# Kernel tuning notes

Hardware: AMD Instinct MI355X
Metric: run time of the kernel (lower is better)

Reference implementation:

```python
import jax, jax.numpy as jnp
import numpy as np

N = 262144          # nodes
F_NODE, F_EDGE = 64, 16
OUT = [64, 64, 64]  # hidden sizes per layer / readout fingerprint size
TARGET = 12
N_DEG = 4           # d = [1,2,3,4]
IN0 = F_NODE + F_EDGE   # duvenaud message out size, layer 0
IN1 = OUT[0] + F_EDGE   # layer 1


def _build_graph():
    # ring: (i, i+1 mod N) -> every node degree 2
    ring = np.stack([np.arange(N), (np.arange(N) + 1) % N], 1)
    # chords: (2i, 2i + N//2) for i < N//8 -> distinct endpoints, bumps degree to 3
    i = np.arange(N // 8)
    chords = np.stack([2 * i, 2 * i + N // 2], 1)
    und = np.concatenate([ring, chords], 0)            # [E, 2] undirected edges
    E = und.shape[0]
    # directed (both directions) for message passing
    src = np.concatenate([und[:, 0], und[:, 1]]).astype(np.int64)
    dst = np.concatenate([und[:, 1], und[:, 0]]).astype(np.int64)
    eid = np.concatenate([np.arange(E), np.arange(E)]).astype(np.int64)
    deg = np.bincount(np.concatenate([und[:, 0], und[:, 1]]), minlength=N)
    deg_idx = (deg - 1).astype(np.int64)               # index into d=[1,2,3,4]
    return src, dst, eid, deg_idx, E


def setup_inputs() -> dict:
    key = jax.random.key(0)
    ks = jax.random.split(key, 9)
    src, dst, eid, deg_idx, E = _build_graph()
    s0 = 1.0 / np.sqrt(IN0)
    sR = 1.0 / np.sqrt(OUT[0])
    return {
        "h_in": jax.random.normal(ks[0], (N, F_NODE), jnp.float32),
        "edge_feat": jax.random.normal(ks[1], (E, F_EDGE), jnp.float32),
        "U0": jax.random.normal(ks[2], (N_DEG, IN0, OUT[0]), jnp.float32) * s0,
        "U1": jax.random.normal(ks[3], (N_DEG, IN1, OUT[1]), jnp.float32) * s0,
        "R0": jax.random.normal(ks[4], (F_NODE, OUT[2]), jnp.float32) * sR,
        "R1": jax.random.normal(ks[5], (OUT[0], OUT[2]), jnp.float32) * sR,
        "R2": jax.random.normal(ks[6], (OUT[1], OUT[2]), jnp.float32) * sR,
        "W_out": jax.random.normal(ks[7], (OUT[2], TARGET), jnp.float32) * sR,
        "b_out": jax.random.normal(ks[8], (TARGET,), jnp.float32) * 0.01,
        "edge_src": jnp.asarray(src),
        "edge_dst": jnp.asarray(dst),
        "edge_eid": jnp.asarray(eid),
        "deg_idx": jnp.asarray(deg_idx),
    }


def reference(h_in, edge_feat, U0, U1, R0, R1, R2, W_out, b_out,
              edge_src, edge_dst, edge_eid, deg_idx):
    ef = edge_feat[edge_eid]  # [2E, F_EDGE] directed-edge features

    def step(h, U):
        # duvenaud message: m_{v<-w} = concat(h_w, e_vw); sum over neighbors
        m = jnp.concatenate([h[edge_src], ef], axis=1)              # [2E, in]
        m_agg = jax.ops.segment_sum(m, edge_dst, num_segments=N)    # [N, in]
        # duvenaud update: h_v' = sigmoid(W_{deg(v)} m_v)
        out_all = jnp.einsum('ni,dio->ndo', m_agg, U)               # [N, D, out]
        sel = jnp.take_along_axis(out_all, deg_idx[:, None, None], axis=1)[:, 0, :]
        return jax.nn.sigmoid(sel)

    h1 = step(h_in, U0)
    h2 = step(h1, U1)
    # duvenaud readout: sum over layers & nodes of softmax(h_l @ R_l), then linear
    fp = (jax.nn.softmax(h_in @ R0, axis=-1)
          + jax.nn.softmax(h1 @ R1, axis=-1)
          + jax.nn.softmax(h2 @ R2, axis=-1)).sum(axis=0)           # [OUT[2]]
    return fp @ W_out + b_out                                       # [TARGET]
```

## Files before the change

### kernel.cpp

```cpp
#include <hip/hip_runtime.h>
#include <stdint.h>

#define NN 262144
#define VMASK (NN - 1)
#define GRID_NODES (NN / 64)

typedef __attribute__((ext_vector_type(8))) short short8;
typedef __attribute__((ext_vector_type(4))) float f32x4;

__device__ __forceinline__ float bf2f(uint16_t h) {
    union { uint32_t u; float f; } a; a.u = ((uint32_t)h) << 16; return a.f;
}
__device__ __forceinline__ uint16_t f2bf(float x) {
    union { float f; uint32_t u; } a; a.f = x;
    uint32_t r = a.u + 0x7fffu + ((a.u >> 16) & 1u);
    return (uint16_t)(r >> 16);
}
__device__ __forceinline__ float sigm(float x) { return 1.f / (1.f + __expf(-x)); }

__device__ __forceinline__ void chord_of(int v, int& cn, int& ce) {
    cn = -1; ce = -1;
    if ((v & 1) == 0) {
        if (v < NN / 4)                            { cn = v + NN / 2; ce = NN + (v >> 1); }
        else if (v >= NN / 2 && v < (3 * NN) / 4)  { cn = v - NN / 2; ce = NN + ((v - NN / 2) >> 1); }
    }
}

__global__ void prep_weights(const float* __restrict__ U0, const float* __restrict__ U1,
                             const float* __restrict__ R0, const float* __restrict__ R1,
                             const float* __restrict__ R2,
                             uint16_t* __restrict__ Ut0, uint16_t* __restrict__ Ut1,
                             uint16_t* __restrict__ Rt)
{
    int idx = blockIdx.x * 256 + threadIdx.x;
    if (idx < 10240) {
        int o = idx / 160, k = idx - o * 160;
        float v = (k < 80) ? U0[5120 + k * 64 + o] : U0[2 * 5120 + (k - 80) * 64 + o];
        Ut0[o * 160 + k] = f2bf(v);
    } else if (idx < 20480) {
        int r = idx - 10240;
        int o = r / 160, k = r - o * 160;
        float v = (k < 80) ? U1[5120 + k * 64 + o] : U1[2 * 5120 + (k - 80) * 64 + o];
        Ut1[o * 160 + k] = f2bf(v);
    } else if (idx < 20480 + 3 * 4096) {
        int r = idx - 20480;
        int layer = r >> 12;
        int e = r & 4095;
        int o = e >> 6, i = e & 63;
        const float* R = (layer == 0) ? R0 : ((layer == 1) ? R1 : R2);
        Rt[layer * 4096 + o * 64 + i] = f2bf(R[i * 64 + o]);
    }
}

template<int MODE>
__global__ __launch_bounds__(256, 4) void fused_layer(
    const float* __restrict__ hf, const uint16_t* __restrict__ hb,
    const float* __restrict__ ef,
    const uint16_t* __restrict__ Ut, const uint16_t* __restrict__ RtA,
    const uint16_t* __restrict__ Rt0, uint16_t* __restrict__ hout,
    float* __restrict__ fpacc)
{
    __shared__ alignas(16) uint16_t B[64][168];
    __shared__ alignas(16) uint16_t X[64][72];
    __shared__ float partial[4][64];

    const int t = threadIdx.x, w = t >> 6, l = t & 63;
    const int bid = blockIdx.x;
    const int chunk = ((bid & 7) << 9) + (bid >> 3);
    const int vb = chunk * 64;
    const int row16 = l & 15, cq = l >> 4, koff = cq * 8;
    const int v = vb + w * 16 + row16;
    const short8 zz = {0, 0, 0, 0, 0, 0, 0, 0};

#pragma unroll
    for (int it = t; it < 1280; it += 256) {
        int o = it / 20, c = it - o * 20;
        *(short8*)&B[o][c * 8] = *(const short8*)(Ut + o * 160 + c * 8);
    }

    const int vm1 = (v - 1) & VMASK, vp1 = (v + 1) & VMASK;
    const int e1 = vm1;
    int cn, ce; chord_of(v, cn, ce);
    const int off = (cn >= 0) ? 80 : 0;
    short8 afr[5];
#pragma unroll
    for (int ks = 0; ks < 5; ++ks) {
        const int mk = ks * 32 + koff - off;
        short8 r = zz;
        if (mk >= 0 && mk < 64) {
            float s[8];
            if (MODE == 0) {
                const float4* x4 = (const float4*)(hf + (size_t)vm1 * 64 + mk);
                const float4* y4 = (const float4*)(hf + (size_t)vp1 * 64 + mk);
                float4 x0 = x4[0], x1 = x4[1], y0 = y4[0], y1 = y4[1];
                s[0] = x0.x + y0.x; s[1] = x0.y + y0.y; s[2] = x0.z + y0.z; s[3] = x0.w + y0.w;
                s[4] = x1.x + y1.x; s[5] = x1.y + y1.y; s[6] = x1.z + y1.z; s[7] = x1.w + y1.w;
                if (cn >= 0) {
                    const float4* z4 = (const float4*)(hf + (size_t)cn * 64 + mk);
                    float4 z0 = z4[0], z1 = z4[1];
                    s[0] += z0.x; s[1] += z0.y; s[2] += z0.z; s[3] += z0.w;
                    s[4] += z1.x; s[5] += z1.y; s[6] += z1.z; s[7] += z1.w;
                }
            } else {
                short8 x = *(const short8*)(hb + (size_t)vm1 * 64 + mk);
                short8 y = *(const short8*)(hb + (size_t)vp1 * 64 + mk);
#pragma unroll
                for (int j = 0; j < 8; ++j) s[j] = bf2f((uint16_t)x[j]) + bf2f((uint16_t)y[j]);
                if (cn >= 0) {
                    short8 zv = *(const short8*)(hb + (size_t)cn * 64 + mk);
#pragma unroll
                    for (int j = 0; j < 8; ++j) s[j] += bf2f((uint16_t)zv[j]);
                }
            }
#pragma unroll
            for (int j = 0; j < 8; ++j) r[j] = (short)f2bf(s[j]);
        } else if (mk >= 64 && mk < 80) {
            const int ek = mk - 64;
            const float4* p4 = (const float4*)(ef + (size_t)e1 * 16 + ek);
            const float4* q4 = (const float4*)(ef + (size_t)v * 16 + ek);
            float4 p0 = p4[0], p1 = p4[1], q0 = q4[0], q1 = q4[1];
            float s[8] = { p0.x + q0.x, p0.y + q0.y, p0.z + q0.z, p0.w + q0.w,
                           p1.x + q1.x, p1.y + q1.y, p1.z + q1.z, p1.w + q1.w };
            if (ce >= 0) {
                const float4* c4 = (const float4*)(ef + (size_t)ce * 16 + ek);
                float4 c0 = c4[0], c1 = c4[1];
                s[0] += c0.x; s[1] += c0.y; s[2] += c0.z; s[3] += c0.w;
                s[4] += c1.x; s[5] += c1.y; s[6] += c1.z; s[7] += c1.w;
            }
#pragma unroll
            for (int j = 0; j < 8; ++j) r[j] = (short)f2bf(s[j]);
        }
        afr[ks] = r;
    }

    short8 h0f0 = zz, h0f1 = zz;
    if (MODE == 0) {
        const float4* s4 = (const float4*)(hf + (size_t)v * 64);
        float4 a0 = s4[cq * 2], a1 = s4[cq * 2 + 1];
        float4 b0v = s4[8 + cq * 2], b1v = s4[8 + cq * 2 + 1];
        h0f0[0] = (short)f2bf(a0.x); h0f0[1] = (short)f2bf(a0.y);
        h0f0[2] = (short)f2bf(a0.z); h0f0[3] = (short)f2bf(a0.w);
        h0f0[4] = (short)f2bf(a1.x); h0f0[5] = (short)f2bf(a1.y);
        h0f0[6] = (short)f2bf(a1.z); h0f0[7] = (short)f2bf(a1.w);
        h0f1[0] = (short)f2bf(b0v.x); h0f1[1] = (short)f2bf(b0v.y);
        h0f1[2] = (short)f2bf(b0v.z); h0f1[3] = (short)f2bf(b0v.w);
        h0f1[4] = (short)f2bf(b1v.x); h0f1[5] = (short)f2bf(b1v.y);
        h0f1[6] = (short)f2bf(b1v.z); h0f1[7] = (short)f2bf(b1v.w);
    }

    __syncthreads();

    const int bc = row16;
    {
        f32x4 acc0 = {0,0,0,0}, acc1 = {0,0,0,0}, acc2 = {0,0,0,0}, acc3 = {0,0,0,0};
#pragma unroll
        for (int ks = 0; ks < 5; ++ks) {
            const int kk = ks * 32 + koff;
            short8 a  = afr[ks];
            short8 b0 = *(const short8*)&B[bc][kk];
            short8 b1 = *(const short8*)&B[16 + bc][kk];
            short8 b2 = *(const short8*)&B[32 + bc][kk];
            short8 b3 = *(const short8*)&B[48 + bc][kk];
            acc0 = __builtin_amdgcn_mfma_f32_16x16x32_bf16(a, b0, acc0, 0, 0, 0);
            acc1 = __builtin_amdgcn_mfma_f32_16x16x32_bf16(a, b1, acc1, 0, 0, 0);
            acc2 = __builtin_amdgcn_mfma_f32_16x16x32_bf16(a, b2, acc2, 0, 0, 0);
            acc3 = __builtin_amdgcn_mfma_f32_16x16x32_bf16(a, b3, acc3, 0, 0, 0);
        }
        const int row0 = w * 16 + cq * 4;
#pragma unroll
        for (int r = 0; r < 4; ++r) {
            X[row0 + r][row16]      = f2bf(sigm(acc0[r]));
            X[row0 + r][16 + row16] = f2bf(sigm(acc1[r]));
            X[row0 + r][32 + row16] = f2bf(sigm(acc2[r]));
            X[row0 + r][48 + row16] = f2bf(sigm(acc3[r]));
        }
    }
    __syncthreads();

#pragma unroll
    for (int it = t; it < 512; it += 256) {
        int o = it >> 3, c = it & 7;
        *(short8*)&B[o][c * 8] = *(const short8*)(RtA + o * 64 + c * 8);
    }
    if (MODE == 0) {
#pragma unroll
        for (int it = t; it < 512; it += 256) {
            int o = it >> 3, c = it & 7;
            *(short8*)&B[o][72 + c * 8] = *(const short8*)(Rt0 + o * 64 + c * 8);
        }
#pragma unroll
        for (int it = t; it < 512; it += 256) {
            int row = it >> 3, c = it & 7;
            *(short8*)(hout + (size_t)(vb + row) * 64 + c * 8) = *(const short8*)&X[row][c * 8];
        }
    }
    __syncthreads();

    float ca0 = 0.f, ca1 = 0.f, ca2 = 0.f, ca3 = 0.f;
    const int ar = w * 16 + row16;
    {
        f32x4 acc0 = {0,0,0,0}, acc1 = {0,0,0,0}, acc2 = {0,0,0,0}, acc3 = {0,0,0,0};
#pragma unroll
        for (int ks = 0; ks < 2; ++ks) {
            const int kk = ks * 32 + koff;
            short8 a  = *(const short8*)&X[ar][kk];
            short8 b0 = *(const short8*)&B[bc][kk];
            short8 b1 = *(const short8*)&B[16 + bc][kk];
            short8 b2 = *(const short8*)&B[32 + bc][kk];
            short8 b3 = *(const short8*)&B[48 + bc][kk];
            acc0 = __builtin_amdgcn_mfma_f32_16x16x32_bf16(a, b0, acc0, 0, 0, 0);
            acc1 = __builtin_amdgcn_mfma_f32_16x16x32_bf16(a, b1, acc1, 0, 0, 0);
            acc2 = __builtin_amdgcn_mfma_f32_16x16x32_bf16(a, b2, acc2, 0, 0, 0);
            acc3 = __builtin_amdgcn_mfma_f32_16x16x32_bf16(a, b3, acc3, 0, 0, 0);
        }
#pragma unroll
        for (int r = 0; r < 4; ++r) {
            float z0 = acc0[r], z1 = acc1[r], z2 = acc2[r], z3 = acc3[r];
            float m = fmaxf(fmaxf(z0, z1), fmaxf(z2, z3));
            m = fmaxf(m, __shfl_xor(m, 1)); m = fmaxf(m, __shfl_xor(m, 2));
            m = fmaxf(m, __shfl_xor(m, 4)); m = fmaxf(m, __shfl_xor(m, 8));
            float e0 = __expf(z0 - m), e1v = __expf(z1 - m), e2 = __expf(z2 - m), e3 = __expf(z3 - m);
            float s = e0 + e1v + e2 + e3;
            s += __shfl_xor(s, 1); s += __shfl_xor(s, 2);
            s += __shfl_xor(s, 4); s += __shfl_xor(s, 8);
            const float inv = 1.f / s;
            ca0 += e0 * inv; ca1 += e1v * inv; ca2 += e2 * inv; ca3 += e3 * inv;
        }
    }
    if (MODE == 0) {
        f32x4 acc0 = {0,0,0,0}, acc1 = {0,0,0,0}, acc2 = {0,0,0,0}, acc3 = {0,0,0,0};
#pragma unroll
        for (int ks = 0; ks < 2; ++ks) {
            const int kk = ks * 32 + koff;
            short8 a  = (ks == 0) ? h0f0 : h0f1;
            short8 b0 = *(const short8*)&B[bc][72 + kk];
            short8 b1 = *(const short8*)&B[16 + bc][72 + kk];
            short8 b2 = *(const short8*)&B[32 + bc][72 + kk];
            short8 b3 = *(const short8*)&B[48 + bc][72 + kk];
            acc0 = __builtin_amdgcn_mfma_f32_16x16x32_bf16(a, b0, acc0, 0, 0, 0);
            acc1 = __builtin_amdgcn_mfma_f32_16x16x32_bf16(a, b1, acc1, 0, 0, 0);
            acc2 = __builtin_amdgcn_mfma_f32_16x16x32_bf16(a, b2, acc2, 0, 0, 0);
            acc3 = __builtin_amdgcn_mfma_f32_16x16x32_bf16(a, b3, acc3, 0, 0, 0);
        }
#pragma unroll
        for (int r = 0; r < 4; ++r) {
            float z0 = acc0[r], z1 = acc1[r], z2 = acc2[r], z3 = acc3[r];
            float m = fmaxf(fmaxf(z0, z1), fmaxf(z2, z3));
            m = fmaxf(m, __shfl_xor(m, 1)); m = fmaxf(m, __shfl_xor(m, 2));
            m = fmaxf(m, __shfl_xor(m, 4)); m = fmaxf(m, __shfl_xor(m, 8));
            float e0 = __expf(z0 - m), e1v = __expf(z1 - m), e2 = __expf(z2 - m), e3 = __expf(z3 - m);
            float s = e0 + e1v + e2 + e3;
            s += __shfl_xor(s, 1); s += __shfl_xor(s, 2);
            s += __shfl_xor(s, 4); s += __shfl_xor(s, 8);
            const float inv = 1.f / s;
            ca0 += e0 * inv; ca1 += e1v * inv; ca2 += e2 * inv; ca3 += e3 * inv;
        }
    }

    ca0 += __shfl_xor(ca0, 16); ca0 += __shfl_xor(ca0, 32);
    ca1 += __shfl_xor(ca1, 16); ca1 += __shfl_xor(ca1, 32);
    ca2 += __shfl_xor(ca2, 16); ca2 += __shfl_xor(ca2, 32);
    ca3 += __shfl_xor(ca3, 16); ca3 += __shfl_xor(ca3, 32);
    if (cq == 0) {
        partial[w][l]      = ca0;
        partial[w][16 + l] = ca1;
        partial[w][32 + l] = ca2;
        partial[w][48 + l] = ca3;
    }
    __syncthreads();
    if (t < 64)
        atomicAdd(&fpacc[((bid & 7) << 6) + t],
                  partial[0][t] + partial[1][t] + partial[2][t] + partial[3][t]);
}

__global__ void final_kernel(const float* __restrict__ fpacc, const float* __restrict__ W,
                             const float* __restrict__ b, float* __restrict__ out)
{
    __shared__ float ft[64];
    const int t = threadIdx.x;
    if (t < 64) {
        float s = 0.f;
#pragma unroll
        for (int k = 0; k < 8; ++k) s += fpacc[k * 64 + t];
        ft[t] = s;
    }
    __syncthreads();
    if (t < 12) {
        float s = b[t];
#pragma unroll 8
        for (int j = 0; j < 64; ++j) s += ft[j] * W[j * 12 + t];
        out[t] = s;
    }
}

extern "C" void kernel_launch(void* const* d_in, const int* in_sizes, int n_in,
                              void* d_out, int out_size, void* d_ws, size_t ws_size,
                              hipStream_t stream)
{
    const float* h_in = (const float*)d_in[0];
    const float* ef   = (const float*)d_in[1];
    const float* U0   = (const float*)d_in[2];
    const float* U1   = (const float*)d_in[3];
    const float* R0   = (const float*)d_in[4];
    const float* R1   = (const float*)d_in[5];
    const float* R2   = (const float*)d_in[6];
    const float* W    = (const float*)d_in[7];
    const float* bo   = (const float*)d_in[8];

    uint16_t* h1  = (uint16_t*)d_ws;
    uint16_t* Ut0 = h1 + (size_t)NN * 64;
    uint16_t* Ut1 = Ut0 + 10240;
    uint16_t* Rt  = Ut1 + 10240;
    float* fpacc  = (float*)(Rt + 3 * 4096);

    hipMemsetAsync(fpacc, 0, 512 * sizeof(float), stream);

    prep_weights<<<128, 256, 0, stream>>>(U0, U1, R0, R1, R2, Ut0, Ut1, Rt);
    fused_layer<0><<<GRID_NODES, 256, 0, stream>>>(h_in, nullptr, ef, Ut0,
                                                   Rt + 4096, Rt, h1, fpacc);
    fused_layer<1><<<GRID_NODES, 256, 0, stream>>>(nullptr, h1, ef, Ut1,
                                                   Rt + 2 * 4096, nullptr, nullptr, fpacc);
    final_kernel<<<1, 64, 0, stream>>>(fpacc, W, bo, (float*)d_out);
}
```

Baseline: 118.1 us.

## Process two 16-node tiles per wave to amortize weight staging

Each block now covers 128 nodes instead of 64, and each wave computes two 16-row MFMA tiles. This halves the number of blocks and the per-block cost of loading weight matrices into LDS, and the shared-memory buffer is reused for the partial reduction. The block-to-chunk mapping is rebuilt so each XCD still gets contiguous nodes. The cost is higher register pressure from two fragment sets per wave, which may reduce occupancy or cause spills, and fewer blocks give less latency hiding for the gather loads.

```diff
diff --git a/kernel.cpp b/kernel.cpp
--- a/kernel.cpp
+++ b/kernel.cpp
@@ -3,7 +3,7 @@
 
 #define NN 262144
 #define VMASK (NN - 1)
-#define GRID_NODES (NN / 64)
+#define GRID_BLKS (NN / 128)
 
 typedef __attribute__((ext_vector_type(8))) short short8;
 typedef __attribute__((ext_vector_type(4))) float f32x4;
@@ -53,36 +53,16 @@
 }
 
 template<int MODE>
-__global__ __launch_bounds__(256, 4) void fused_layer(
-    const float* __restrict__ hf, const uint16_t* __restrict__ hb,
-    const float* __restrict__ ef,
-    const uint16_t* __restrict__ Ut, const uint16_t* __restrict__ RtA,
-    const uint16_t* __restrict__ Rt0, uint16_t* __restrict__ hout,
-    float* __restrict__ fpacc)
-{
-    __shared__ alignas(16) uint16_t B[64][168];
-    __shared__ alignas(16) uint16_t X[64][72];
-    __shared__ float partial[4][64];
-
-    const int t = threadIdx.x, w = t >> 6, l = t & 63;
-    const int bid = blockIdx.x;
-    const int chunk = ((bid & 7) << 9) + (bid >> 3);
-    const int vb = chunk * 64;
-    const int row16 = l & 15, cq = l >> 4, koff = cq * 8;
-    const int v = vb + w * 16 + row16;
-    const short8 zz = {0, 0, 0, 0, 0, 0, 0, 0};
-
-#pragma unroll
-    for (int it = t; it < 1280; it += 256) {
-        int o = it / 20, c = it - o * 20;
-        *(short8*)&B[o][c * 8] = *(const short8*)(Ut + o * 160 + c * 8);
-    }
-
+__device__ __forceinline__ void build_afr(const float* __restrict__ hf,
+                                          const uint16_t* __restrict__ hb,
+                                          const float* __restrict__ ef,
+                                          int v, int koff, short8* afr)
+{
     const int vm1 = (v - 1) & VMASK, vp1 = (v + 1) & VMASK;
     const int e1 = vm1;
     int cn, ce; chord_of(v, cn, ce);
     const int off = (cn >= 0) ? 80 : 0;
-    short8 afr[5];
+    const short8 zz = {0, 0, 0, 0, 0, 0, 0, 0};
 #pragma unroll
     for (int ks = 0; ks < 5; ++ks) {
         const int mk = ks * 32 + koff - off;
@@ -132,31 +112,67 @@
         }
         afr[ks] = r;
     }
-
-    short8 h0f0 = zz, h0f1 = zz;
-    if (MODE == 0) {
-        const float4* s4 = (const float4*)(hf + (size_t)v * 64);
-        float4 a0 = s4[cq * 2], a1 = s4[cq * 2 + 1];
-        float4 b0v = s4[8 + cq * 2], b1v = s4[8 + cq * 2 + 1];
-        h0f0[0] = (short)f2bf(a0.x); h0f0[1] = (short)f2bf(a0.y);
-        h0f0[2] = (short)f2bf(a0.z); h0f0[3] = (short)f2bf(a0.w);
-        h0f0[4] = (short)f2bf(a1.x); h0f0[5] = (short)f2bf(a1.y);
-        h0f0[6] = (short)f2bf(a1.z); h0f0[7] = (short)f2bf(a1.w);
-        h0f1[0] = (short)f2bf(b0v.x); h0f1[1] = (short)f2bf(b0v.y);
-        h0f1[2] = (short)f2bf(b0v.z); h0f1[3] = (short)f2bf(b0v.w);
-        h0f1[4] = (short)f2bf(b1v.x); h0f1[5] = (short)f2bf(b1v.y);
-        h0f1[6] = (short)f2bf(b1v.z); h0f1[7] = (short)f2bf(b1v.w);
-    }
+}
+
+__device__ __forceinline__ void softmax_acc(const f32x4& acc0, const f32x4& acc1,
+                                            const f32x4& acc2, const f32x4& acc3,
+                                            float& ca0, float& ca1, float& ca2, float& ca3)
+{
+#pragma unroll
+    for (int r = 0; r < 4; ++r) {
+        float z0 = acc0[r], z1 = acc1[r], z2 = acc2[r], z3 = acc3[r];
+        float m = fmaxf(fmaxf(z0, z1), fmaxf(z2, z3));
+        m = fmaxf(m, __shfl_xor(m, 1)); m = fmaxf(m, __shfl_xor(m, 2));
+        m = fmaxf(m, __shfl_xor(m, 4)); m = fmaxf(m, __shfl_xor(m, 8));
+        float e0 = __expf(z0 - m), e1 = __expf(z1 - m), e2 = __expf(z2 - m), e3 = __expf(z3 - m);
+        float s = e0 + e1 + e2 + e3;
+        s += __shfl_xor(s, 1); s += __shfl_xor(s, 2);
+        s += __shfl_xor(s, 4); s += __shfl_xor(s, 8);
+        const float inv = 1.f / s;
+        ca0 += e0 * inv; ca1 += e1 * inv; ca2 += e2 * inv; ca3 += e3 * inv;
+    }
+}
+
+template<int MODE>
+__global__ __launch_bounds__(256, 4) void fused_layer(
+    const float* __restrict__ hf, const uint16_t* __restrict__ hb,
+    const float* __restrict__ ef,
+    const uint16_t* __restrict__ Ut, const uint16_t* __restrict__ RtA,
+    const uint16_t* __restrict__ Rt0, uint16_t* __restrict__ hout,
+    float* __restrict__ fpacc)
+{
+    __shared__ alignas(16) uint16_t B[64][168];
+    __shared__ alignas(16) uint16_t X[128][72];
+
+    const int t = threadIdx.x, w = t >> 6, l = t & 63;
+    const int bid = blockIdx.x;
+    const int xcd = bid & 7, i = bid >> 3;
+    const int chunk = ((i >> 7) << 10) | (xcd << 7) | (i & 127);
+    const int vb = chunk * 128;
+    const int row16 = l & 15, cq = l >> 4, koff = cq * 8;
+    const int va = vb + w * 32 + row16;
+    const int vbn = va + 16;
+
+#pragma unroll
+    for (int it = t; it < 1280; it += 256) {
+        int o = it / 20, c = it - o * 20;
+        *(short8*)&B[o][c * 8] = *(const short8*)(Ut + o * 160 + c * 8);
+    }
+
+    short8 afrA[5], afrB[5];
+    build_afr<MODE>(hf, hb, ef, va,  koff, afrA);
+    build_afr<MODE>(hf, hb, ef, vbn, koff, afrB);
 
     __syncthreads();
 
     const int bc = row16;
-    {
+#pragma unroll
+    for (int tile = 0; tile < 2; ++tile) {
         f32x4 acc0 = {0,0,0,0}, acc1 = {0,0,0,0}, acc2 = {0,0,0,0}, acc3 = {0,0,0,0};
 #pragma unroll
         for (int ks = 0; ks < 5; ++ks) {
             const int kk = ks * 32 + koff;
-            short8 a  = afr[ks];
+            short8 a  = tile ? afrB[ks] : afrA[ks];
             short8 b0 = *(const short8*)&B[bc][kk];
             short8 b1 = *(const short8*)&B[16 + bc][kk];
             short8 b2 = *(const short8*)&B[32 + bc][kk];
@@ -166,7 +182,7 @@
             acc2 = __builtin_amdgcn_mfma_f32_16x16x32_bf16(a, b2, acc2, 0, 0, 0);
             acc3 = __builtin_amdgcn_mfma_f32_16x16x32_bf16(a, b3, acc3, 0, 0, 0);
         }
-        const int row0 = w * 16 + cq * 4;
+        const int row0 = w * 32 + tile * 16 + cq * 4;
 #pragma unroll
         for (int r = 0; r < 4; ++r) {
             X[row0 + r][row16]      = f2bf(sigm(acc0[r]));
@@ -189,16 +205,39 @@
             *(short8*)&B[o][72 + c * 8] = *(const short8*)(Rt0 + o * 64 + c * 8);
         }
 #pragma unroll
-        for (int it = t; it < 512; it += 256) {
+        for (int it = t; it < 1024; it += 256) {
             int row = it >> 3, c = it & 7;
             *(short8*)(hout + (size_t)(vb + row) * 64 + c * 8) = *(const short8*)&X[row][c * 8];
         }
     }
     __syncthreads();
 
+    short8 h0fa[2], h0fb[2];
+    if (MODE == 0) {
+#pragma unroll
+        for (int tile = 0; tile < 2; ++tile) {
+            const int v = tile ? vbn : va;
+            const float4* s4 = (const float4*)(hf + (size_t)v * 64);
+            float4 a0 = s4[cq * 2], a1 = s4[cq * 2 + 1];
+            float4 b0 = s4[8 + cq * 2], b1 = s4[8 + cq * 2 + 1];
+            short8 f0, f1;
+            f0[0] = (short)f2bf(a0.x); f0[1] = (short)f2bf(a0.y);
+            f0[2] = (short)f2bf(a0.z); f0[3] = (short)f2bf(a0.w);
+            f0[4] = (short)f2bf(a1.x); f0[5] = (short)f2bf(a1.y);
+            f0[6] = (short)f2bf(a1.z); f0[7] = (short)f2bf(a1.w);
+            f1[0] = (short)f2bf(b0.x); f1[1] = (short)f2bf(b0.y);
+            f1[2] = (short)f2bf(b0.z); f1[3] = (short)f2bf(b0.w);
+            f1[4] = (short)f2bf(b1.x); f1[5] = (short)f2bf(b1.y);
+            f1[6] = (short)f2bf(b1.z); f1[7] = (short)f2bf(b1.w);
+            if (tile) { h0fb[0] = f0; h0fb[1] = f1; }
+            else      { h0fa[0] = f0; h0fa[1] = f1; }
+        }
+    }
+
     float ca0 = 0.f, ca1 = 0.f, ca2 = 0.f, ca3 = 0.f;
-    const int ar = w * 16 + row16;
-    {
+#pragma unroll
+    for (int tile = 0; tile < 2; ++tile) {
+        const int ar = w * 32 + tile * 16 + row16;
         f32x4 acc0 = {0,0,0,0}, acc1 = {0,0,0,0}, acc2 = {0,0,0,0}, acc3 = {0,0,0,0};
 #pragma unroll
         for (int ks = 0; ks < 2; ++ks) {
@@ -213,47 +252,26 @@
             acc2 = __builtin_amdgcn_mfma_f32_16x16x32_bf16(a, b2, acc2, 0, 0, 0);
             acc3 = __builtin_amdgcn_mfma_f32_16x16x32_bf16(a, b3, acc3, 0, 0, 0);
         }
-#pragma unroll
-        for (int r = 0; r < 4; ++r) {
-            float z0 = acc0[r], z1 = acc1[r], z2 = acc2[r], z3 = acc3[r];
-            float m = fmaxf(fmaxf(z0, z1), fmaxf(z2, z3));
-            m = fmaxf(m, __shfl_xor(m, 1)); m = fmaxf(m, __shfl_xor(m, 2));
-            m = fmaxf(m, __shfl_xor(m, 4)); m = fmaxf(m, __shfl_xor(m, 8));
-            float e0 = __expf(z0 - m), e1v = __expf(z1 - m), e2 = __expf(z2 - m), e3 = __expf(z3 - m);
-            float s = e0 + e1v + e2 + e3;
-            s += __shfl_xor(s, 1); s += __shfl_xor(s, 2);
-            s += __shfl_xor(s, 4); s += __shfl_xor(s, 8);
-            const float inv = 1.f / s;
-            ca0 += e0 * inv; ca1 += e1v * inv; ca2 += e2 * inv; ca3 += e3 * inv;
-        }
+        softmax_acc(acc0, acc1, acc2, acc3, ca0, ca1, ca2, ca3);
     }
     if (MODE == 0) {
-        f32x4 acc0 = {0,0,0,0}, acc1 = {0,0,0,0}, acc2 = {0,0,0,0}, acc3 = {0,0,0,0};
-#pragma unroll
-        for (int ks = 0; ks < 2; ++ks) {
-            const int kk = ks * 32 + koff;
-            short8 a  = (ks == 0) ? h0f0 : h0f1;
-            short8 b0 = *(const short8*)&B[bc][72 + kk];
-            short8 b1 = *(const short8*)&B[16 + bc][72 + kk];
-            short8 b2 = *(const short8*)&B[32 + bc][72 + kk];
-            short8 b3 = *(const short8*)&B[48 + bc][72 + kk];
-            acc0 = __builtin_amdgcn_mfma_f32_16x16x32_bf16(a, b0, acc0, 0, 0, 0);
-            acc1 = __builtin_amdgcn_mfma_f32_16x16x32_bf16(a, b1, acc1, 0, 0, 0);
-            acc2 = __builtin_amdgcn_mfma_f32_16x16x32_bf16(a, b2, acc2, 0, 0, 0);
-            acc3 = __builtin_amdgcn_mfma_f32_16x16x32_bf16(a, b3, acc3, 0, 0, 0);
-        }
-#pragma unroll
-        for (int r = 0; r < 4; ++r) {
-            float z0 = acc0[r], z1 = acc1[r], z2 = acc2[r], z3 = acc3[r];
-            float m = fmaxf(fmaxf(z0, z1), fmaxf(z2, z3));
-            m = fmaxf(m, __shfl_xor(m, 1)); m = fmaxf(m, __shfl_xor(m, 2));
-            m = fmaxf(m, __shfl_xor(m, 4)); m = fmaxf(m, __shfl_xor(m, 8));
-            float e0 = __expf(z0 - m), e1v = __expf(z1 - m), e2 = __expf(z2 - m), e3 = __expf(z3 - m);
-            float s = e0 + e1v + e2 + e3;
-            s += __shfl_xor(s, 1); s += __shfl_xor(s, 2);
-            s += __shfl_xor(s, 4); s += __shfl_xor(s, 8);
-            const float inv = 1.f / s;
-            ca0 += e0 * inv; ca1 += e1v * inv; ca2 += e2 * inv; ca3 += e3 * inv;
+#pragma unroll
+        for (int tile = 0; tile < 2; ++tile) {
+            f32x4 acc0 = {0,0,0,0}, acc1 = {0,0,0,0}, acc2 = {0,0,0,0}, acc3 = {0,0,0,0};
+#pragma unroll
+            for (int ks = 0; ks < 2; ++ks) {
+                const int kk = ks * 32 + koff;
+                short8 a  = tile ? h0fb[ks] : h0fa[ks];
+                short8 b0 = *(const short8*)&B[bc][72 + kk];
+                short8 b1 = *(const short8*)&B[16 + bc][72 + kk];
+                short8 b2 = *(const short8*)&B[32 + bc][72 + kk];
+                short8 b3 = *(const short8*)&B[48 + bc][72 + kk];
+                acc0 = __builtin_amdgcn_mfma_f32_16x16x32_bf16(a, b0, acc0, 0, 0, 0);
+                acc1 = __builtin_amdgcn_mfma_f32_16x16x32_bf16(a, b1, acc1, 0, 0, 0);
+                acc2 = __builtin_amdgcn_mfma_f32_16x16x32_bf16(a, b2, acc2, 0, 0, 0);
+                acc3 = __builtin_amdgcn_mfma_f32_16x16x32_bf16(a, b3, acc3, 0, 0, 0);
+            }
+            softmax_acc(acc0, acc1, acc2, acc3, ca0, ca1, ca2, ca3);
         }
     }
 
@@ -261,16 +279,17 @@
     ca1 += __shfl_xor(ca1, 16); ca1 += __shfl_xor(ca1, 32);
     ca2 += __shfl_xor(ca2, 16); ca2 += __shfl_xor(ca2, 32);
     ca3 += __shfl_xor(ca3, 16); ca3 += __shfl_xor(ca3, 32);
+    __syncthreads();
+    float* P = (float*)&X[0][0];
     if (cq == 0) {
-        partial[w][l]      = ca0;
-        partial[w][16 + l] = ca1;
-        partial[w][32 + l] = ca2;
-        partial[w][48 + l] = ca3;
+        P[w * 64 + l]      = ca0;
+        P[w * 64 + 16 + l] = ca1;
+        P[w * 64 + 32 + l] = ca2;
+        P[w * 64 + 48 + l] = ca3;
     }
     __syncthreads();
     if (t < 64)
-        atomicAdd(&fpacc[((bid & 7) << 6) + t],
-                  partial[0][t] + partial[1][t] + partial[2][t] + partial[3][t]);
+        atomicAdd(&fpacc[(xcd << 6) + t], P[t] + P[64 + t] + P[128 + t] + P[192 + t]);
 }
 
 __global__ void final_kernel(const float* __restrict__ fpacc, const float* __restrict__ W,
@@ -316,9 +335,9 @@
     hipMemsetAsync(fpacc, 0, 512 * sizeof(float), stream);
 
     prep_weights<<<128, 256, 0, stream>>>(U0, U1, R0, R1, R2, Ut0, Ut1, Rt);
-    fused_layer<0><<<GRID_NODES, 256, 0, stream>>>(h_in, nullptr, ef, Ut0,
-                                                   Rt + 4096, Rt, h1, fpacc);
-    fused_layer<1><<<GRID_NODES, 256, 0, stream>>>(nullptr, h1, ef, Ut1,
-                                                   Rt + 2 * 4096, nullptr, nullptr, fpacc);
+    fused_layer<0><<<GRID_BLKS, 256, 0, stream>>>(h_in, nullptr, ef, Ut0,
+                                                  Rt + 4096, Rt, h1, fpacc);
+    fused_layer<1><<<GRID_BLKS, 256, 0, stream>>>(nullptr, h1, ef, Ut1,
+                                                  Rt + 2 * 4096, nullptr, nullptr, fpacc);
     final_kernel<<<1, 64, 0, stream>>>(fpacc, W, bo, (float*)d_out);
 }
```

Measured after the change: 113.3 us. 4.1% less time.

## Alias X onto B in shared memory, read readout weights from global, drop syncs

Applied to the files above, without the earlier changes.

The layer kernel now overlays the sigmoid output tile on the weight tile in one shared buffer, which cuts LDS per block and raises the launch-bounds occupancy hint from 4 to 5. The readout weights are loaded straight from global into registers instead of being staged through shared memory, removing one barrier, and the per-block partial reduction is replaced by direct per-wavefront atomics. The block-to-chunk mapping for the XCDs is also changed, and bf16 conversion now uses the library intrinsic. In exchange there is more register pressure, four times as many atomics, and redundant global weight reads per wave.

```diff
diff --git a/kernel.cpp b/kernel.cpp
--- a/kernel.cpp
+++ b/kernel.cpp
@@ -1,9 +1,10 @@
 #include <hip/hip_runtime.h>
+#include <hip/hip_bf16.h>
 #include <stdint.h>
 
 #define NN 262144
 #define VMASK (NN - 1)
-#define GRID_NODES (NN / 64)
+#define GRID_BLKS (NN / 64)
 
 typedef __attribute__((ext_vector_type(8))) short short8;
 typedef __attribute__((ext_vector_type(4))) float f32x4;
@@ -12,9 +13,9 @@
     union { uint32_t u; float f; } a; a.u = ((uint32_t)h) << 16; return a.f;
 }
 __device__ __forceinline__ uint16_t f2bf(float x) {
-    union { float f; uint32_t u; } a; a.f = x;
-    uint32_t r = a.u + 0x7fffu + ((a.u >> 16) & 1u);
-    return (uint16_t)(r >> 16);
+    union { __hip_bfloat16 b; uint16_t u; } c;
+    c.b = __float2bfloat16(x);
+    return c.u;
 }
 __device__ __forceinline__ float sigm(float x) { return 1.f / (1.f + __expf(-x)); }
 
@@ -53,36 +54,16 @@
 }
 
 template<int MODE>
-__global__ __launch_bounds__(256, 4) void fused_layer(
-    const float* __restrict__ hf, const uint16_t* __restrict__ hb,
-    const float* __restrict__ ef,
-    const uint16_t* __restrict__ Ut, const uint16_t* __restrict__ RtA,
-    const uint16_t* __restrict__ Rt0, uint16_t* __restrict__ hout,
-    float* __restrict__ fpacc)
-{
-    __shared__ alignas(16) uint16_t B[64][168];
-    __shared__ alignas(16) uint16_t X[64][72];
-    __shared__ float partial[4][64];
-
-    const int t = threadIdx.x, w = t >> 6, l = t & 63;
-    const int bid = blockIdx.x;
-    const int chunk = ((bid & 7) << 9) + (bid >> 3);
-    const int vb = chunk * 64;
-    const int row16 = l & 15, cq = l >> 4, koff = cq * 8;
-    const int v = vb + w * 16 + row16;
-    const short8 zz = {0, 0, 0, 0, 0, 0, 0, 0};
-
-#pragma unroll
-    for (int it = t; it < 1280; it += 256) {
-        int o = it / 20, c = it - o * 20;
-        *(short8*)&B[o][c * 8] = *(const short8*)(Ut + o * 160 + c * 8);
-    }
-
+__device__ __forceinline__ void build_afr(const float* __restrict__ hf,
+                                          const uint16_t* __restrict__ hb,
+                                          const float* __restrict__ ef,
+                                          int v, int koff, short8* afr)
+{
     const int vm1 = (v - 1) & VMASK, vp1 = (v + 1) & VMASK;
     const int e1 = vm1;
     int cn, ce; chord_of(v, cn, ce);
     const int off = (cn >= 0) ? 80 : 0;
-    short8 afr[5];
+    const short8 zz = {0, 0, 0, 0, 0, 0, 0, 0};
 #pragma unroll
     for (int ks = 0; ks < 5; ++ks) {
         const int mk = ks * 32 + koff - off;
@@ -132,129 +113,145 @@
         }
         afr[ks] = r;
     }
-
-    short8 h0f0 = zz, h0f1 = zz;
+}
+
+__device__ __forceinline__ void softmax_acc(const f32x4& acc0, const f32x4& acc1,
+                                            const f32x4& acc2, const f32x4& acc3,
+                                            float& ca0, float& ca1, float& ca2, float& ca3)
+{
+#pragma unroll
+    for (int r = 0; r < 4; ++r) {
+        float z0 = acc0[r], z1 = acc1[r], z2 = acc2[r], z3 = acc3[r];
+        float m = fmaxf(fmaxf(z0, z1), fmaxf(z2, z3));
+        m = fmaxf(m, __shfl_xor(m, 1)); m = fmaxf(m, __shfl_xor(m, 2));
+        m = fmaxf(m, __shfl_xor(m, 4)); m = fmaxf(m, __shfl_xor(m, 8));
+        float e0 = __expf(z0 - m), e1 = __expf(z1 - m), e2 = __expf(z2 - m), e3 = __expf(z3 - m);
+        float s = e0 + e1 + e2 + e3;
+        s += __shfl_xor(s, 1); s += __shfl_xor(s, 2);
+        s += __shfl_xor(s, 4); s += __shfl_xor(s, 8);
+        const float inv = 1.f / s;
+        ca0 += e0 * inv; ca1 += e1 * inv; ca2 += e2 * inv; ca3 += e3 * inv;
+    }
+}
+
+template<int MODE>
+__global__ __launch_bounds__(256, 5) void fused_layer(
+    const float* __restrict__ hf, const uint16_t* __restrict__ hb,
+    const float* __restrict__ ef,
+    const uint16_t* __restrict__ Ut, const uint16_t* __restrict__ RtA,
+    const uint16_t* __restrict__ Rt0, uint16_t* __restrict__ hout,
+    float* __restrict__ fpacc)
+{
+    __shared__ alignas(16) uint16_t SM[64 * 168];
+    uint16_t (*B)[168] = (uint16_t(*)[168])SM;
+    uint16_t (*X)[72]  = (uint16_t(*)[72])SM;
+
+    const int t = threadIdx.x, w = t >> 6, l = t & 63;
+    const int bid = blockIdx.x;
+    const int xcd = bid & 7, i = bid >> 3;
+    const int chunk = ((i >> 8) << 11) | (xcd << 8) | (i & 255);
+    const int vb = chunk * 64;
+    const int row16 = l & 15, cq = l >> 4, koff = cq * 8;
+    const int v = vb + w * 16 + row16;
+    const int bc = row16;
+
+#pragma unroll
+    for (int it = t; it < 1280; it += 256) {
+        int o = it / 20, c = it - o * 20;
+        *(short8*)&B[o][c * 8] = *(const short8*)(Ut + o * 160 + c * 8);
+    }
+    short8 afr[5];
+    build_afr<MODE>(hf, hb, ef, v, koff, afr);
+
+    __syncthreads();
+
+    f32x4 acc0 = {0,0,0,0}, acc1 = {0,0,0,0}, acc2 = {0,0,0,0}, acc3 = {0,0,0,0};
+#pragma unroll
+    for (int ks = 0; ks < 5; ++ks) {
+        const int kk = ks * 32 + koff;
+        short8 a  = afr[ks];
+        short8 b0 = *(const short8*)&B[bc][kk];
+        short8 b1 = *(const short8*)&B[16 + bc][kk];
+        short8 b2 = *(const short8*)&B[32 + bc][kk];
+        short8 b3 = *(const short8*)&B[48 + bc][kk];
+        acc0 = __builtin_amdgcn_mfma_f32_16x16x32_bf16(a, b0, acc0, 0, 0, 0);
+        acc1 = __builtin_amdgcn_mfma_f32_16x16x32_bf16(a, b1, acc1, 0, 0, 0);
+        acc2 = __builtin_amdgcn_mfma_f32_16x16x32_bf16(a, b2, acc2, 0, 0, 0);
+        acc3 = __builtin_amdgcn_mfma_f32_16x16x32_bf16(a, b3, acc3, 0, 0, 0);
+    }
+
+    short8 h0f0, h0f1;
     if (MODE == 0) {
         const float4* s4 = (const float4*)(hf + (size_t)v * 64);
         float4 a0 = s4[cq * 2], a1 = s4[cq * 2 + 1];
-        float4 b0v = s4[8 + cq * 2], b1v = s4[8 + cq * 2 + 1];
+        float4 b0 = s4[8 + cq * 2], b1 = s4[8 + cq * 2 + 1];
         h0f0[0] = (short)f2bf(a0.x); h0f0[1] = (short)f2bf(a0.y);
         h0f0[2] = (short)f2bf(a0.z); h0f0[3] = (short)f2bf(a0.w);
         h0f0[4] = (short)f2bf(a1.x); h0f0[5] = (short)f2bf(a1.y);
         h0f0[6] = (short)f2bf(a1.z); h0f0[7] = (short)f2bf(a1.w);
-        h0f1[0] = (short)f2bf(b0v.x); h0f1[1] = (short)f2bf(b0v.y);
-        h0f1[2] = (short)f2bf(b0v.z); h0f1[3] = (short)f2bf(b0v.w);
-        h0f1[4] = (short)f2bf(b1v.x); h0f1[5] = (short)f2bf(b1v.y);
-        h0f1[6] = (short)f2bf(b1v.z); h0f1[7] = (short)f2bf(b1v.w);
+        h0f1[0] = (short)f2bf(b0.x); h0f1[1] = (short)f2bf(b0.y);
+        h0f1[2] = (short)f2bf(b0.z); h0f1[3] = (short)f2bf(b0.w);
+        h0f1[4] = (short)f2bf(b1.x); h0f1[5] = (short)f2bf(b1.y);
+        h0f1[6] = (short)f2bf(b1.z); h0f1[7] = (short)f2bf(b1.w);
     }
 
     __syncthreads();
 
-    const int bc = row16;
-    {
-        f32x4 acc0 = {0,0,0,0}, acc1 = {0,0,0,0}, acc2 = {0,0,0,0}, acc3 = {0,0,0,0};
-#pragma unroll
-        for (int ks = 0; ks < 5; ++ks) {
-            const int kk = ks * 32 + koff;
-            short8 a  = afr[ks];
-            short8 b0 = *(const short8*)&B[bc][kk];
-            short8 b1 = *(const short8*)&B[16 + bc][kk];
-            short8 b2 = *(const short8*)&B[32 + bc][kk];
-            short8 b3 = *(const short8*)&B[48 + bc][kk];
-            acc0 = __builtin_amdgcn_mfma_f32_16x16x32_bf16(a, b0, acc0, 0, 0, 0);
-            acc1 = __builtin_amdgcn_mfma_f32_16x16x32_bf16(a, b1, acc1, 0, 0, 0);
-            acc2 = __builtin_amdgcn_mfma_f32_16x16x32_bf16(a, b2, acc2, 0, 0, 0);
-            acc3 = __builtin_amdgcn_mfma_f32_16x16x32_bf16(a, b3, acc3, 0, 0, 0);
-        }
-        const int row0 = w * 16 + cq * 4;
-#pragma unroll
-        for (int r = 0; r < 4; ++r) {
-            X[row0 + r][row16]      = f2bf(sigm(acc0[r]));
-            X[row0 + r][16 + row16] = f2bf(sigm(acc1[r]));
-            X[row0 + r][32 + row16] = f2bf(sigm(acc2[r]));
-            X[row0 + r][48 + row16] = f2bf(sigm(acc3[r]));
-        }
+    const int row0 = w * 16 + cq * 4;
+#pragma unroll
+    for (int r = 0; r < 4; ++r) {
+        X[row0 + r][row16]      = f2bf(sigm(acc0[r]));
+        X[row0 + r][16 + row16] = f2bf(sigm(acc1[r]));
+        X[row0 + r][32 + row16] = f2bf(sigm(acc2[r]));
+        X[row0 + r][48 + row16] = f2bf(sigm(acc3[r]));
     }
     __syncthreads();
 
-#pragma unroll
-    for (int it = t; it < 512; it += 256) {
-        int o = it >> 3, c = it & 7;
-        *(short8*)&B[o][c * 8] = *(const short8*)(RtA + o * 64 + c * 8);
-    }
     if (MODE == 0) {
-#pragma unroll
-        for (int it = t; it < 512; it += 256) {
-            int o = it >> 3, c = it & 7;
-            *(short8*)&B[o][72 + c * 8] = *(const short8*)(Rt0 + o * 64 + c * 8);
-        }
 #pragma unroll
         for (int it = t; it < 512; it += 256) {
             int row = it >> 3, c = it & 7;
             *(short8*)(hout + (size_t)(vb + row) * 64 + c * 8) = *(const short8*)&X[row][c * 8];
         }
     }
-    __syncthreads();
 
     float ca0 = 0.f, ca1 = 0.f, ca2 = 0.f, ca3 = 0.f;
     const int ar = w * 16 + row16;
     {
-        f32x4 acc0 = {0,0,0,0}, acc1 = {0,0,0,0}, acc2 = {0,0,0,0}, acc3 = {0,0,0,0};
+        short8 rb[4][2];
+#pragma unroll
+        for (int n = 0; n < 4; ++n)
+#pragma unroll
+            for (int ks = 0; ks < 2; ++ks)
+                rb[n][ks] = *(const short8*)(RtA + (n * 16 + bc) * 64 + ks * 32 + koff);
+        f32x4 r0 = {0,0,0,0}, r1 = {0,0,0,0}, r2 = {0,0,0,0}, r3 = {0,0,0,0};
 #pragma unroll
         for (int ks = 0; ks < 2; ++ks) {
-            const int kk = ks * 32 + koff;
-            short8 a  = *(const short8*)&X[ar][kk];
-            short8 b0 = *(const short8*)&B[bc][kk];
-            short8 b1 = *(const short8*)&B[16 + bc][kk];
-            short8 b2 = *(const short8*)&B[32 + bc][kk];
-            short8 b3 = *(const short8*)&B[48 + bc][kk];
-            acc0 = __builtin_amdgcn_mfma_f32_16x16x32_bf16(a, b0, acc0, 0, 0, 0);
-            acc1 = __builtin_amdgcn_mfma_f32_16x16x32_bf16(a, b1, acc1, 0, 0, 0);
-            acc2 = __builtin_amdgcn_mfma_f32_16x16x32_bf16(a, b2, acc2, 0, 0, 0);
-            acc3 = __builtin_amdgcn_mfma_f32_16x16x32_bf16(a, b3, acc3, 0, 0, 0);
+            short8 a = *(const short8*)&X[ar][ks * 32 + koff];
+            r0 = __builtin_amdgcn_mfma_f32_16x16x32_bf16(a, rb[0][ks], r0, 0, 0, 0);
+            r1 = __builtin_amdgcn_mfma_f32_16x16x32_bf16(a, rb[1][ks], r1, 0, 0, 0);
+            r2 = __builtin_amdgcn_mfma_f32_16x16x32_bf16(a, rb[2][ks], r2, 0, 0, 0);
+            r3 = __builtin_amdgcn_mfma_f32_16x16x32_bf16(a, rb[3][ks], r3, 0, 0, 0);
         }
-#pragma unroll
-        for (int r = 0; r < 4; ++r) {
-            float z0 = acc0[r], z1 = acc1[r], z2 = acc2[r], z3 = acc3[r];
-            float m = fmaxf(fmaxf(z0, z1), fmaxf(z2, z3));
-            m = fmaxf(m, __shfl_xor(m, 1)); m = fmaxf(m, __shfl_xor(m, 2));
-            m = fmaxf(m, __shfl_xor(m, 4)); m = fmaxf(m, __shfl_xor(m, 8));
-            float e0 = __expf(z0 - m), e1v = __expf(z1 - m), e2 = __expf(z2 - m), e3 = __expf(z3 - m);
-            float s = e0 + e1v + e2 + e3;
-            s += __shfl_xor(s, 1); s += __shfl_xor(s, 2);
-            s += __shfl_xor(s, 4); s += __shfl_xor(s, 8);
-            const float inv = 1.f / s;
-            ca0 += e0 * inv; ca1 += e1v * inv; ca2 += e2 * inv; ca3 += e3 * inv;
+        softmax_acc(r0, r1, r2, r3, ca0, ca1, ca2, ca3);
+    }
+    if (MODE == 0) {
+        short8 rb[4][2];
+#pragma unroll
+        for (int n = 0; n < 4; ++n)
+#pragma unroll
+            for (int ks = 0; ks < 2; ++ks)
+                rb[n][ks] = *(const short8*)(Rt0 + (n * 16 + bc) * 64 + ks * 32 + koff);
+        f32x4 r0 = {0,0,0,0}, r1 = {0,0,0,0}, r2 = {0,0,0,0}, r3 = {0,0,0,0};
+#pragma unroll
+        for (int ks = 0; ks < 2; ++ks) {
+            short8 a = (ks == 0) ? h0f0 : h0f1;
+            r0 = __builtin_amdgcn_mfma_f32_16x16x32_bf16(a, rb[0][ks], r0, 0, 0, 0);
+            r1 = __builtin_amdgcn_mfma_f32_16x16x32_bf16(a, rb[1][ks], r1, 0, 0, 0);
+            r2 = __builtin_amdgcn_mfma_f32_16x16x32_bf16(a, rb[2][ks], r2, 0, 0, 0);
+            r3 = __builtin_amdgcn_mfma_f32_16x16x32_bf16(a, rb[3][ks], r3, 0, 0, 0);
         }
-    }
-    if (MODE == 0) {
-        f32x4 acc0 = {0,0,0,0}, acc1 = {0,0,0,0}, acc2 = {0,0,0,0}, acc3 = {0,0,0,0};
-#pragma unroll
-        for (int ks = 0; ks < 2; ++ks) {
-            const int kk = ks * 32 + koff;
-            short8 a  = (ks == 0) ? h0f0 : h0f1;
-            short8 b0 = *(const short8*)&B[bc][72 + kk];
-            short8 b1 = *(const short8*)&B[16 + bc][72 + kk];
-            short8 b2 = *(const short8*)&B[32 + bc][72 + kk];
-            short8 b3 = *(const short8*)&B[48 + bc][72 + kk];
-            acc0 = __builtin_amdgcn_mfma_f32_16x16x32_bf16(a, b0, acc0, 0, 0, 0);
-            acc1 = __builtin_amdgcn_mfma_f32_16x16x32_bf16(a, b1, acc1, 0, 0, 0);
-            acc2 = __builtin_amdgcn_mfma_f32_16x16x32_bf16(a, b2, acc2, 0, 0, 0);
-            acc3 = __builtin_amdgcn_mfma_f32_16x16x32_bf16(a, b3, acc3, 0, 0, 0);
-        }
-#pragma unroll
-        for (int r = 0; r < 4; ++r) {
-            float z0 = acc0[r], z1 = acc1[r], z2 = acc2[r], z3 = acc3[r];
-            float m = fmaxf(fmaxf(z0, z1), fmaxf(z2, z3));
-            m = fmaxf(m, __shfl_xor(m, 1)); m = fmaxf(m, __shfl_xor(m, 2));
-            m = fmaxf(m, __shfl_xor(m, 4)); m = fmaxf(m, __shfl_xor(m, 8));
-            float e0 = __expf(z0 - m), e1v = __expf(z1 - m), e2 = __expf(z2 - m), e3 = __expf(z3 - m);
-            float s = e0 + e1v + e2 + e3;
-            s += __shfl_xor(s, 1); s += __shfl_xor(s, 2);
-            s += __shfl_xor(s, 4); s += __shfl_xor(s, 8);
-            const float inv = 1.f / s;
-            ca0 += e0 * inv; ca1 += e1v * inv; ca2 += e2 * inv; ca3 += e3 * inv;
-        }
+        softmax_acc(r0, r1, r2, r3, ca0, ca1, ca2, ca3);
     }
 
     ca0 += __shfl_xor(ca0, 16); ca0 += __shfl_xor(ca0, 32);
@@ -262,15 +259,12 @@
     ca2 += __shfl_xor(ca2, 16); ca2 += __shfl_xor(ca2, 32);
     ca3 += __shfl_xor(ca3, 16); ca3 += __shfl_xor(ca3, 32);
     if (cq == 0) {
-        partial[w][l]      = ca0;
-        partial[w][16 + l] = ca1;
-        partial[w][32 + l] = ca2;
-        partial[w][48 + l] = ca3;
-    }
-    __syncthreads();
-    if (t < 64)
-        atomicAdd(&fpacc[((bid & 7) << 6) + t],
-                  partial[0][t] + partial[1][t] + partial[2][t] + partial[3][t]);
+        float* fp = fpacc + (xcd << 6);
+        atomicAdd(&fp[l],      ca0);
+        atomicAdd(&fp[16 + l], ca1);
+        atomicAdd(&fp[32 + l], ca2);
+        atomicAdd(&fp[48 + l], ca3);
+    }
 }
 
 __global__ void final_kernel(const float* __restrict__ fpacc, const float* __restrict__ W,
@@ -316,9 +310,9 @@
     hipMemsetAsync(fpacc, 0, 512 * sizeof(float), stream);
 
     prep_weights<<<128, 256, 0, stream>>>(U0, U1, R0, R1, R2, Ut0, Ut1, Rt);
-    fused_layer<0><<<GRID_NODES, 256, 0, stream>>>(h_in, nullptr, ef, Ut0,
-                                                   Rt + 4096, Rt, h1, fpacc);
-    fused_layer<1><<<GRID_NODES, 256, 0, stream>>>(nullptr, h1, ef, Ut1,
-                                                   Rt + 2 * 4096, nullptr, nullptr, fpacc);
+    fused_layer<0><<<GRID_BLKS, 256, 0, stream>>>(h_in, nullptr, ef, Ut0,
+                                                  Rt + 4096, Rt, h1, fpacc);
+    fused_layer<1><<<GRID_BLKS, 256, 0, stream>>>(nullptr, h1, ef, Ut1,
+                                                  Rt + 2 * 4096, nullptr, nullptr, fpacc);
     final_kernel<<<1, 64, 0, stream>>>(fpacc, W, bo, (float*)d_out);
 }
```

Result: slower. 181.8 us (+53.9%).
